# Performance work log

Hardware: AMD Instinct MI355X
Metric: run time of the kernel (lower is better)

The kernel has to match this reference:

```python
import jax, jax.numpy as jnp
import numpy as np

NUM_HEADS = 8
EPS = 1e-12  # F.normalize default eps


def setup_inputs() -> dict:
    key = jax.random.key(0)
    ks = jax.random.split(key, 6)
    dim = 64
    b, h, w = 1, 64, 64
    x = jax.random.normal(ks[0], (b, dim, h, w), dtype=jnp.float32)
    y = jax.random.normal(ks[1], (b, dim, h, w), dtype=jnp.float32)
    # 1x1 conv weights (kernel dims squeezed), kaiming-ish scale
    s = 1.0 / np.sqrt(dim)
    w_q = jax.random.normal(ks[2], (dim, dim), dtype=jnp.float32) * s
    w_kv = jax.random.normal(ks[3], (2 * dim, dim), dtype=jnp.float32) * s
    w_out = jax.random.normal(ks[4], (dim, dim), dtype=jnp.float32) * s
    temperature = jnp.ones((NUM_HEADS, 1, 1), dtype=jnp.float32)
    return {"x": x, "y": y, "w_q": w_q, "w_kv": w_kv, "w_out": w_out,
            "temperature": temperature}


def _l2norm(t):
    n = jnp.sqrt(jnp.sum(t * t, axis=-1, keepdims=True))
    return t / jnp.maximum(n, EPS)


def reference(x, y, w_q, w_kv, w_out, temperature):
    b, c, h, w = x.shape
    hd = c // NUM_HEADS  # per-head channel dim
    # 1x1 convs == channel matmuls
    q = jnp.einsum('oc,bchw->bohw', w_q, x)
    kv = jnp.einsum('oc,bchw->bohw', w_kv, y)
    k, v = jnp.split(kv, 2, axis=1)
    def to_heads(t):  # b (head c) h w -> b head (h w) c
        return t.reshape(b, NUM_HEADS, hd, h * w).transpose(0, 1, 3, 2)
    q, k, v = to_heads(q), to_heads(k), to_heads(v)
    q = _l2norm(q)
    k = _l2norm(k)
    # cosine-similarity logits scaled by learned per-head temperature
    attn = jnp.einsum('bhnc,bhmc->bhnm', q, k) * temperature[None]
    attn = jax.nn.softmax(attn, axis=-1)
    out = jnp.einsum('bhnm,bhmc->bhnc', attn, v)
    out = out.transpose(0, 1, 3, 2).reshape(b, c, h, w)
    return jnp.einsum('oc,bchw->bohw', w_out, out)
```

## Files before the change

kernel.cpp:

```cpp
#include <hip/hip_runtime.h>
#include <hip/hip_bf16.h>

#define DIM 64
#define N 4096
#define NH 8
#define HD 8
#define KPW 512

typedef __hip_bfloat16 bf16;
typedef __attribute__((ext_vector_type(8))) short short8;
typedef __attribute__((ext_vector_type(16))) float f32x16;
#define MFMA32 __builtin_amdgcn_mfma_f32_32x32x16_bf16

__device__ __forceinline__ float b2f(bf16 v) { return __bfloat162float(v); }

__device__ __forceinline__ bool is_bf16_mode(const void* temp) {
    return (((const unsigned*)temp)[0] & 0xFFFFu) != 0u;
}
__device__ __forceinline__ float ldany(const void* p, int i, bool isbf) {
    return isbf ? b2f(((const bf16*)p)[i]) : ((const float*)p)[i];
}
__device__ __forceinline__ unsigned pk(float a, float b) {
    union { __hip_bfloat162 h; unsigned u; } z;
    z.h = __float22bfloat162_rn(make_float2(a, b));
    return z.u;
}

__global__ __launch_bounds__(256) void proj_qkv(
    const void* __restrict__ x, const void* __restrict__ y,
    const void* __restrict__ w_q, const void* __restrict__ w_kv,
    const void* __restrict__ temp,
    ushort* __restrict__ qg, ushort* __restrict__ kg, ushort* __restrict__ vg)
{
    const bool isbf = is_bf16_mode(temp);
    const int mode = blockIdx.y;
    const int px = blockIdx.x * 64 + (threadIdx.x & 63);
    const int grp = threadIdx.x >> 6;
    const void* in = (mode == 0) ? x : y;
    const void* w  = (mode == 0) ? w_q : w_kv;
    const int woff = (mode == 2) ? DIM * DIM : 0;

    __shared__ float wl[DIM * DIM];
    for (int i = threadIdx.x; i < DIM * DIM; i += 256) {
        int o = i >> 6, c = i & 63;
        wl[c * DIM + o] = ldany(w, woff + i, isbf);
    }
    __syncthreads();

    float acc[16];
#pragma unroll
    for (int o = 0; o < 16; o++) acc[o] = 0.f;

#pragma unroll 8
    for (int c = 0; c < DIM; c++) {
        float xv = ldany(in, c * N + px, isbf);
        const float* wrow = &wl[c * DIM + grp * 16];
#pragma unroll
        for (int o = 0; o < 16; o += 4) {
            float4 wv = *(const float4*)&wrow[o];
            acc[o + 0] = fmaf(wv.x, xv, acc[o + 0]);
            acc[o + 1] = fmaf(wv.y, xv, acc[o + 1]);
            acc[o + 2] = fmaf(wv.z, xv, acc[o + 2]);
            acc[o + 3] = fmaf(wv.w, xv, acc[o + 3]);
        }
    }

    ushort* dst = (mode == 0) ? qg : (mode == 1 ? kg : vg);
#pragma unroll
    for (int hh = 0; hh < 2; hh++) {
        int h = grp * 2 + hh;
        float* a = &acc[hh * 8];
        if (mode < 2) {
            float s = 0.f;
#pragma unroll
            for (int c = 0; c < HD; c++) s = fmaf(a[c], a[c], s);
            float inv = 1.0f / fmaxf(sqrtf(s), 1e-12f);
            if (mode == 0)
                inv *= ldany(temp, h, isbf) * 1.44269504088896340736f;
#pragma unroll
            for (int c = 0; c < HD; c++) a[c] *= inv;
        }
        uint4 pkt;
        pkt.x = pk(a[0], a[1]); pkt.y = pk(a[2], a[3]);
        pkt.z = pk(a[4], a[5]); pkt.w = pk(a[6], a[7]);
        *(uint4*)(dst + ((size_t)h * N + px) * 8) = pkt;
    }
}

__global__ __launch_bounds__(512) void attn_mfma(
    const ushort* __restrict__ qg, const ushort* __restrict__ kg,
    const ushort* __restrict__ vg, float* __restrict__ og)
{
    const int h = blockIdx.y;
    const int qbase = blockIdx.x * 32;
    const int tid = threadIdx.x;
    const int wv = tid >> 6;
    const int lane = tid & 63;
    const int lr = lane & 31;
    const int g  = lane >> 5;

    __shared__ __align__(16) ushort vt[8 * 612];
    __shared__ __align__(16) ushort zsh[64];
    __shared__ float pbuf[8 * 256];
    __shared__ float lbuf[8 * 32];
    __shared__ float linv[32];

    ushort* vtw = vt + wv * 612;
    zsh[lane] = 0;
    vtw[8 * 68 + lane] = 0x3F80;

    const ushort* qgh = qg + (size_t)h * N * 8;
    short8 qf = {0, 0, 0, 0, 0, 0, 0, 0};
    if (lane < 32) {
        uint4 t4 = *(const uint4*)(qgh + (size_t)(qbase + lr) * 8);
        unsigned* qu = (unsigned*)&qf;
        qu[0] = t4.x; qu[1] = t4.y; qu[2] = t4.z; qu[3] = t4.w;
    }

    const int swp = (lr & ~12) | ((lr & 4) << 1) | ((lr & 8) >> 1);
    const ushort* vp = (lr <= 8) ? (vtw + lr * 68 + g * 8) : &zsh[0];

    const ushort* kgh = kg + (size_t)h * N * 8;
    const ushort* vgh = vg + (size_t)h * N * 8;

    f32x16 zz = {0,0,0,0,0,0,0,0,0,0,0,0,0,0,0,0};
    f32x16 o2 = {0,0,0,0,0,0,0,0,0,0,0,0,0,0,0,0};

    for (int st = 0; st < KPW / 64; st++) {
        const int kb = wv * KPW + st * 64;

        uint4 v4 = *(const uint4*)(vgh + (size_t)(kb + lane) * 8);
        unsigned vw[4] = {v4.x, v4.y, v4.z, v4.w};
#pragma unroll
        for (int c = 0; c < 4; c++) {
            vtw[(2 * c + 0) * 68 + lane] = (ushort)(vw[c] & 0xFFFFu);
            vtw[(2 * c + 1) * 68 + lane] = (ushort)(vw[c] >> 16);
        }

        uint4 k40 = make_uint4(0, 0, 0, 0), k41 = make_uint4(0, 0, 0, 0);
        if (lane < 32) {
            k40 = *(const uint4*)(kgh + (size_t)(kb + swp) * 8);
            k41 = *(const uint4*)(kgh + (size_t)(kb + 32 + swp) * 8);
        }

#pragma unroll
        for (int s = 0; s < 2; s++) {
            short8 kf;
            {
                uint4 ks = s ? k41 : k40;
                unsigned* ku = (unsigned*)&kf;
                ku[0] = ks.x; ku[1] = ks.y; ku[2] = ks.z; ku[3] = ks.w;
            }
            f32x16 d1 = MFMA32(kf, qf, zz, 0, 0, 0);

            short8 p0, p1;
            unsigned* p0u = (unsigned*)&p0;
            unsigned* p1u = (unsigned*)&p1;
#pragma unroll
            for (int w = 0; w < 4; w++) {
                p0u[w] = pk(__builtin_amdgcn_exp2f(d1[2 * w]),
                            __builtin_amdgcn_exp2f(d1[2 * w + 1]));
                p1u[w] = pk(__builtin_amdgcn_exp2f(d1[8 + 2 * w]),
                            __builtin_amdgcn_exp2f(d1[8 + 2 * w + 1]));
            }
#pragma unroll
            for (int t = 0; t < 2; t++) {
                const ushort* vpt = vp + s * 32 + t * 16;
                short8 vf;
                uint2 va = *(const uint2*)(vpt + 0);
                uint2 vb = *(const uint2*)(vpt + 4);
                unsigned* vu = (unsigned*)&vf;
                vu[0] = va.x; vu[1] = va.y; vu[2] = vb.x; vu[3] = vb.y;
                o2 = MFMA32(vf, t == 0 ? p0 : p1, o2, 0, 0, 0);
            }
        }
    }

    *(float4*)&pbuf[wv * 256 + lr * 8 + g * 4] =
        make_float4(o2[0], o2[1], o2[2], o2[3]);
    if (g == 0) lbuf[wv * 32 + lr] = o2[4];
    __syncthreads();

    float sum = 0.f;
    if (tid < 256) {
        const int q = tid >> 3, ch = tid & 7;
#pragma unroll
        for (int w = 0; w < 8; w++) sum += pbuf[w * 256 + q * 8 + ch];
    } else if (tid < 288) {
        const int q = tid - 256;
        float L = 0.f;
#pragma unroll
        for (int w = 0; w < 8; w++) L += lbuf[w * 32 + q];
        linv[q] = 1.0f / L;
    }
    __syncthreads();

    if (tid < 256) {
        const int q = tid >> 3, ch = tid & 7;
        og[((size_t)h * N + qbase + q) * 8 + ch] = sum * linv[q];
    }
}

__global__ __launch_bounds__(256) void out_proj(
    const float* __restrict__ og, const void* __restrict__ w_out,
    const void* __restrict__ temp, void* __restrict__ out)
{
    const bool isbf = is_bf16_mode(temp);
    const int px = blockIdx.x * 64 + (threadIdx.x & 63);
    const int grp = threadIdx.x >> 6;

    __shared__ float wl[DIM * DIM];
    for (int i = threadIdx.x; i < DIM * DIM; i += 256) {
        int o = i >> 6, c = i & 63;
        wl[c * DIM + o] = ldany(w_out, i, isbf);
    }
    __syncthreads();

    float acc[16];
#pragma unroll
    for (int o = 0; o < 16; o++) acc[o] = 0.f;

#pragma unroll
    for (int h = 0; h < NH; h++) {
        float4 lo = *(const float4*)(og + ((size_t)h * N + px) * 8 + 0);
        float4 hi = *(const float4*)(og + ((size_t)h * N + px) * 8 + 4);
        float vals[8] = {lo.x, lo.y, lo.z, lo.w, hi.x, hi.y, hi.z, hi.w};
#pragma unroll
        for (int cc = 0; cc < 8; cc++) {
            float xv = vals[cc];
            const float* wrow = &wl[(h * HD + cc) * DIM + grp * 16];
#pragma unroll
            for (int o = 0; o < 16; o += 4) {
                float4 wv = *(const float4*)&wrow[o];
                acc[o + 0] = fmaf(wv.x, xv, acc[o + 0]);
                acc[o + 1] = fmaf(wv.y, xv, acc[o + 1]);
                acc[o + 2] = fmaf(wv.z, xv, acc[o + 2]);
                acc[o + 3] = fmaf(wv.w, xv, acc[o + 3]);
            }
        }
    }
    if (isbf) {
        bf16* ob = (bf16*)out;
#pragma unroll
        for (int o = 0; o < 16; o++) ob[(grp * 16 + o) * N + px] = __float2bfloat16(acc[o]);
    } else {
        float* of = (float*)out;
#pragma unroll
        for (int o = 0; o < 16; o++) of[(grp * 16 + o) * N + px] = acc[o];
    }
}

extern "C" void kernel_launch(void* const* d_in, const int* in_sizes, int n_in,
                              void* d_out, int out_size, void* d_ws, size_t ws_size,
                              hipStream_t stream)
{
    const void* x     = d_in[0];
    const void* y     = d_in[1];
    const void* w_q   = d_in[2];
    const void* w_kv  = d_in[3];
    const void* w_out = d_in[4];
    const void* temp  = d_in[5];

    ushort* qg = (ushort*)d_ws;
    ushort* kg = qg + (size_t)NH * N * 8;
    ushort* vg = kg + (size_t)NH * N * 8;
    float*  og = (float*)(vg + (size_t)NH * N * 8);

    proj_qkv<<<dim3(N / 64, 3), 256, 0, stream>>>(x, y, w_q, w_kv, temp, qg, kg, vg);
    attn_mfma<<<dim3(N / 32, NH), 512, 0, stream>>>(qg, kg, vg, og);
    out_proj<<<dim3(N / 64), 256, 0, stream>>>(og, w_out, temp, d_out);
}
```

Baseline: 109.6 us.

## Double-buffer K/V loads in attention and widen projection kernel grids

The QKV projection now gives each thread one head of eight outputs and launches twice as many blocks. The attention kernel prefetches the next K/V tile into registers and double-buffers the transposed V in LDS, so global loads overlap with MFMA work. The attention output is stored pixel-major (pixel × 64 channels), which lets the output projection read contiguous float4 rows, compute four outputs per thread and run on four times as many blocks. The trade-offs are more redundant weight staging into LDS per block, extra LDS and registers in the attention kernel, and less coalesced per-thread reads in out_proj.

```diff
diff --git a/kernel.cpp b/kernel.cpp
--- a/kernel.cpp
+++ b/kernel.cpp
@@ -34,8 +34,8 @@
 {
     const bool isbf = is_bf16_mode(temp);
     const int mode = blockIdx.y;
-    const int px = blockIdx.x * 64 + (threadIdx.x & 63);
-    const int grp = threadIdx.x >> 6;
+    const int px = blockIdx.x * 32 + (threadIdx.x & 31);
+    const int grp = threadIdx.x >> 5;
     const void* in = (mode == 0) ? x : y;
     const void* w  = (mode == 0) ? w_q : w_kv;
     const int woff = (mode == 2) ? DIM * DIM : 0;
@@ -47,44 +47,38 @@
     }
     __syncthreads();
 
-    float acc[16];
-#pragma unroll
-    for (int o = 0; o < 16; o++) acc[o] = 0.f;
+    float a[8];
+#pragma unroll
+    for (int o = 0; o < 8; o++) a[o] = 0.f;
 
 #pragma unroll 8
     for (int c = 0; c < DIM; c++) {
         float xv = ldany(in, c * N + px, isbf);
-        const float* wrow = &wl[c * DIM + grp * 16];
-#pragma unroll
-        for (int o = 0; o < 16; o += 4) {
-            float4 wv = *(const float4*)&wrow[o];
-            acc[o + 0] = fmaf(wv.x, xv, acc[o + 0]);
-            acc[o + 1] = fmaf(wv.y, xv, acc[o + 1]);
-            acc[o + 2] = fmaf(wv.z, xv, acc[o + 2]);
-            acc[o + 3] = fmaf(wv.w, xv, acc[o + 3]);
-        }
+        const float* wrow = &wl[c * DIM + grp * 8];
+        float4 w0 = *(const float4*)&wrow[0];
+        float4 w1 = *(const float4*)&wrow[4];
+        a[0] = fmaf(w0.x, xv, a[0]); a[1] = fmaf(w0.y, xv, a[1]);
+        a[2] = fmaf(w0.z, xv, a[2]); a[3] = fmaf(w0.w, xv, a[3]);
+        a[4] = fmaf(w1.x, xv, a[4]); a[5] = fmaf(w1.y, xv, a[5]);
+        a[6] = fmaf(w1.z, xv, a[6]); a[7] = fmaf(w1.w, xv, a[7]);
+    }
+
+    if (mode < 2) {
+        float s = 0.f;
+#pragma unroll
+        for (int c = 0; c < 8; c++) s = fmaf(a[c], a[c], s);
+        float inv = 1.0f / fmaxf(sqrtf(s), 1e-12f);
+        if (mode == 0)
+            inv *= ldany(temp, grp, isbf) * 1.44269504088896340736f;
+#pragma unroll
+        for (int c = 0; c < 8; c++) a[c] *= inv;
     }
 
     ushort* dst = (mode == 0) ? qg : (mode == 1 ? kg : vg);
-#pragma unroll
-    for (int hh = 0; hh < 2; hh++) {
-        int h = grp * 2 + hh;
-        float* a = &acc[hh * 8];
-        if (mode < 2) {
-            float s = 0.f;
-#pragma unroll
-            for (int c = 0; c < HD; c++) s = fmaf(a[c], a[c], s);
-            float inv = 1.0f / fmaxf(sqrtf(s), 1e-12f);
-            if (mode == 0)
-                inv *= ldany(temp, h, isbf) * 1.44269504088896340736f;
-#pragma unroll
-            for (int c = 0; c < HD; c++) a[c] *= inv;
-        }
-        uint4 pkt;
-        pkt.x = pk(a[0], a[1]); pkt.y = pk(a[2], a[3]);
-        pkt.z = pk(a[4], a[5]); pkt.w = pk(a[6], a[7]);
-        *(uint4*)(dst + ((size_t)h * N + px) * 8) = pkt;
-    }
+    uint4 pkt;
+    pkt.x = pk(a[0], a[1]); pkt.y = pk(a[2], a[3]);
+    pkt.z = pk(a[4], a[5]); pkt.w = pk(a[6], a[7]);
+    *(uint4*)(dst + ((size_t)grp * N + px) * 8) = pkt;
 }
 
 __global__ __launch_bounds__(512) void attn_mfma(
@@ -99,15 +93,16 @@
     const int lr = lane & 31;
     const int g  = lane >> 5;
 
-    __shared__ __align__(16) ushort vt[8 * 612];
+    __shared__ __align__(16) ushort vt[8 * 2 * 612];
     __shared__ __align__(16) ushort zsh[64];
     __shared__ float pbuf[8 * 256];
     __shared__ float lbuf[8 * 32];
     __shared__ float linv[32];
 
-    ushort* vtw = vt + wv * 612;
+    ushort* vtw = vt + wv * 2 * 612;
     zsh[lane] = 0;
     vtw[8 * 68 + lane] = 0x3F80;
+    vtw[612 + 8 * 68 + lane] = 0x3F80;
 
     const ushort* qgh = qg + (size_t)h * N * 8;
     short8 qf = {0, 0, 0, 0, 0, 0, 0, 0};
@@ -118,7 +113,8 @@
     }
 
     const int swp = (lr & ~12) | ((lr & 4) << 1) | ((lr & 8) >> 1);
-    const ushort* vp = (lr <= 8) ? (vtw + lr * 68 + g * 8) : &zsh[0];
+    const ushort* vp0 = (lr <= 8) ? (vtw + lr * 68 + g * 8) : &zsh[0];
+    const int vstep = (lr <= 8) ? 612 : 0;
 
     const ushort* kgh = kg + (size_t)h * N * 8;
     const ushort* vgh = vg + (size_t)h * N * 8;
@@ -126,23 +122,36 @@
     f32x16 zz = {0,0,0,0,0,0,0,0,0,0,0,0,0,0,0,0};
     f32x16 o2 = {0,0,0,0,0,0,0,0,0,0,0,0,0,0,0,0};
 
+    const int kb0 = wv * KPW;
+    uint4 v4 = *(const uint4*)(vgh + (size_t)(kb0 + lane) * 8);
+    uint4 k40 = make_uint4(0, 0, 0, 0), k41 = make_uint4(0, 0, 0, 0);
+    if (lane < 32) {
+        k40 = *(const uint4*)(kgh + (size_t)(kb0 + swp) * 8);
+        k41 = *(const uint4*)(kgh + (size_t)(kb0 + 32 + swp) * 8);
+    }
+
     for (int st = 0; st < KPW / 64; st++) {
-        const int kb = wv * KPW + st * 64;
-
-        uint4 v4 = *(const uint4*)(vgh + (size_t)(kb + lane) * 8);
-        unsigned vw[4] = {v4.x, v4.y, v4.z, v4.w};
-#pragma unroll
-        for (int c = 0; c < 4; c++) {
-            vtw[(2 * c + 0) * 68 + lane] = (ushort)(vw[c] & 0xFFFFu);
-            vtw[(2 * c + 1) * 68 + lane] = (ushort)(vw[c] >> 16);
-        }
-
-        uint4 k40 = make_uint4(0, 0, 0, 0), k41 = make_uint4(0, 0, 0, 0);
+        const int buf = st & 1;
+        ushort* vtc = vtw + buf * 612;
+
+        {
+            unsigned vw[4] = {v4.x, v4.y, v4.z, v4.w};
+#pragma unroll
+            for (int c = 0; c < 4; c++) {
+                vtc[(2 * c + 0) * 68 + lane] = (ushort)(vw[c] & 0xFFFFu);
+                vtc[(2 * c + 1) * 68 + lane] = (ushort)(vw[c] >> 16);
+            }
+        }
+
+        const int kbn = wv * KPW + ((st < KPW / 64 - 1) ? (st + 1) * 64 : st * 64);
+        uint4 v4n = *(const uint4*)(vgh + (size_t)(kbn + lane) * 8);
+        uint4 k40n = make_uint4(0, 0, 0, 0), k41n = make_uint4(0, 0, 0, 0);
         if (lane < 32) {
-            k40 = *(const uint4*)(kgh + (size_t)(kb + swp) * 8);
-            k41 = *(const uint4*)(kgh + (size_t)(kb + 32 + swp) * 8);
-        }
-
+            k40n = *(const uint4*)(kgh + (size_t)(kbn + swp) * 8);
+            k41n = *(const uint4*)(kgh + (size_t)(kbn + 32 + swp) * 8);
+        }
+
+        const ushort* vp = vp0 + buf * vstep;
 #pragma unroll
         for (int s = 0; s < 2; s++) {
             short8 kf;
@@ -174,6 +183,7 @@
                 o2 = MFMA32(vf, t == 0 ? p0 : p1, o2, 0, 0, 0);
             }
         }
+        v4 = v4n; k40 = k40n; k41 = k41n;
     }
 
     *(float4*)&pbuf[wv * 256 + lr * 8 + g * 4] =
@@ -197,7 +207,7 @@
 
     if (tid < 256) {
         const int q = tid >> 3, ch = tid & 7;
-        og[((size_t)h * N + qbase + q) * 8 + ch] = sum * linv[q];
+        og[(size_t)(qbase + q) * DIM + h * 8 + ch] = sum * linv[q];
     }
 }
 
@@ -206,8 +216,8 @@
     const void* __restrict__ temp, void* __restrict__ out)
 {
     const bool isbf = is_bf16_mode(temp);
-    const int px = blockIdx.x * 64 + (threadIdx.x & 63);
-    const int grp = threadIdx.x >> 6;
+    const int px = blockIdx.x * 16 + (threadIdx.x & 15);
+    const int grp = threadIdx.x >> 4;
 
     __shared__ float wl[DIM * DIM];
     for (int i = threadIdx.x; i < DIM * DIM; i += 256) {
@@ -216,37 +226,33 @@
     }
     __syncthreads();
 
-    float acc[16];
-#pragma unroll
-    for (int o = 0; o < 16; o++) acc[o] = 0.f;
-
-#pragma unroll
-    for (int h = 0; h < NH; h++) {
-        float4 lo = *(const float4*)(og + ((size_t)h * N + px) * 8 + 0);
-        float4 hi = *(const float4*)(og + ((size_t)h * N + px) * 8 + 4);
-        float vals[8] = {lo.x, lo.y, lo.z, lo.w, hi.x, hi.y, hi.z, hi.w};
-#pragma unroll
-        for (int cc = 0; cc < 8; cc++) {
-            float xv = vals[cc];
-            const float* wrow = &wl[(h * HD + cc) * DIM + grp * 16];
-#pragma unroll
-            for (int o = 0; o < 16; o += 4) {
-                float4 wv = *(const float4*)&wrow[o];
-                acc[o + 0] = fmaf(wv.x, xv, acc[o + 0]);
-                acc[o + 1] = fmaf(wv.y, xv, acc[o + 1]);
-                acc[o + 2] = fmaf(wv.z, xv, acc[o + 2]);
-                acc[o + 3] = fmaf(wv.w, xv, acc[o + 3]);
-            }
-        }
-    }
+    float a0 = 0.f, a1 = 0.f, a2 = 0.f, a3 = 0.f;
+    const float4* og4 = (const float4*)(og + (size_t)px * DIM);
+#pragma unroll 4
+    for (int c4 = 0; c4 < DIM / 4; c4++) {
+        float4 ov = og4[c4];
+        float xs[4] = {ov.x, ov.y, ov.z, ov.w};
+#pragma unroll
+        for (int u = 0; u < 4; u++) {
+            const float* wrow = &wl[(c4 * 4 + u) * DIM + grp * 4];
+            float4 wv = *(const float4*)wrow;
+            a0 = fmaf(wv.x, xs[u], a0); a1 = fmaf(wv.y, xs[u], a1);
+            a2 = fmaf(wv.z, xs[u], a2); a3 = fmaf(wv.w, xs[u], a3);
+        }
+    }
+
     if (isbf) {
         bf16* ob = (bf16*)out;
-#pragma unroll
-        for (int o = 0; o < 16; o++) ob[(grp * 16 + o) * N + px] = __float2bfloat16(acc[o]);
+        ob[(grp * 4 + 0) * N + px] = __float2bfloat16(a0);
+        ob[(grp * 4 + 1) * N + px] = __float2bfloat16(a1);
+        ob[(grp * 4 + 2) * N + px] = __float2bfloat16(a2);
+        ob[(grp * 4 + 3) * N + px] = __float2bfloat16(a3);
     } else {
         float* of = (float*)out;
-#pragma unroll
-        for (int o = 0; o < 16; o++) of[(grp * 16 + o) * N + px] = acc[o];
+        of[(grp * 4 + 0) * N + px] = a0;
+        of[(grp * 4 + 1) * N + px] = a1;
+        of[(grp * 4 + 2) * N + px] = a2;
+        of[(grp * 4 + 3) * N + px] = a3;
     }
 }
 
@@ -266,7 +272,7 @@
     ushort* vg = kg + (size_t)NH * N * 8;
     float*  og = (float*)(vg + (size_t)NH * N * 8);
 
-    proj_qkv<<<dim3(N / 64, 3), 256, 0, stream>>>(x, y, w_q, w_kv, temp, qg, kg, vg);
+    proj_qkv<<<dim3(N / 32, 3), 256, 0, stream>>>(x, y, w_q, w_kv, temp, qg, kg, vg);
     attn_mfma<<<dim3(N / 32, NH), 512, 0, stream>>>(qg, kg, vg, og);
-    out_proj<<<dim3(N / 64), 256, 0, stream>>>(og, w_out, temp, d_out);
-}
+    out_proj<<<dim3(N / 16), 256, 0, stream>>>(og, w_out, temp, d_out);
+}
```

Result: faster. 103.8 us (-5.3%).
